# Kernel optimization log

Hardware: AMD Instinct MI355X
Metric: run time of the kernel (lower is better)

Reference implementation:

```python
import jax, jax.numpy as jnp
import numpy as np

B, T, C, H = 8, 2048, 1024, 1024
SCALE = 1.0 / np.sqrt(H).astype(np.float32)


def setup_inputs() -> dict:
    key = jax.random.key(0)
    kx, kq, kk, kv = jax.random.split(key, 4)
    x = jax.random.normal(kx, (B, T, C), dtype=jnp.float32)
    # Linear(C -> H, bias=False): store weights as [C, H] so y = x @ W
    Wq = jax.random.normal(kq, (C, H), dtype=jnp.float32) * (1.0 / np.sqrt(C))
    Wk = jax.random.normal(kk, (C, H), dtype=jnp.float32) * (1.0 / np.sqrt(C))
    Wv = jax.random.normal(kv, (C, H), dtype=jnp.float32) * (1.0 / np.sqrt(C))
    return {"x": x, "Wq": Wq, "Wk": Wk, "Wv": Wv}


def reference(x, Wq, Wk, Wv):
    # Projections
    Q = jnp.einsum('btc,ch->bth', x, Wq)
    K = jnp.einsum('btc,ch->bth', x, Wk)
    V = jnp.einsum('btc,ch->bth', x, Wv)
    t = x.shape[1]
    # Scaled dot-product scores with causal mask
    attn = jnp.einsum('bqh,bkh->bqk', Q, K) * SCALE  # [B,T,T]
    causal = jnp.tril(jnp.ones((t, t), dtype=bool))
    attn = jnp.where(causal, attn, -jnp.inf)
    scores = jax.nn.softmax(attn, axis=-1)
    # dropout p=0.0 (eval/deterministic) -> identity
    out = jnp.einsum('bqk,bkh->bqh', scores, V)
    return out
```

## Files before the change

kernel.cpp:

```cpp
#include <hip/hip_runtime.h>


#define BM 128
#define BN 128
#define BK 32

typedef __attribute__((ext_vector_type(8))) __bf16 bf16x8;
typedef __attribute__((ext_vector_type(4))) float floatx4;

__device__ __forceinline__ unsigned short f2bf(float f) {
  unsigned int u = __float_as_uint(f);
  u += 0x7fffu + ((u >> 16) & 1u);
  return (unsigned short)(u >> 16);
}
__device__ __forceinline__ float bf2f(unsigned short s) {
  return __uint_as_float(((unsigned int)s) << 16);
}

__device__ __forceinline__ void gload_lds16(const unsigned short* g, unsigned short* l) {
  __builtin_amdgcn_global_load_lds(
      (const __attribute__((address_space(1))) void*)g,
      (__attribute__((address_space(3))) void*)l,
      16, 0, 0);
}


__device__ __forceinline__ void gemm_mainloop(
    const unsigned short* __restrict__ A, int lda,
    const unsigned short* __restrict__ Bt, int ldb,
    int m0, int n0, int kTiles,
    unsigned short* As, unsigned short* Bs,
    floatx4 (&acc)[4][4])
{
  const int tid  = threadIdx.x;
  const int wave = tid >> 6;
  const int lane = tid & 63;
  const int wr = wave >> 1;
  const int wc = wave & 1;

  const int c0 = wave * 2;
  const int c1 = c0 + 1;
  const int r0 = c0 * 16 + (lane >> 2);
  const int r1 = c1 * 16 + (lane >> 2);
  const int ck = (lane & 3) * 8;

  const unsigned short* pA0 = A  + (size_t)(m0 + r0) * lda + ck;
  const unsigned short* pA1 = A  + (size_t)(m0 + r1) * lda + ck;
  const unsigned short* pB0 = Bt + (size_t)(n0 + r0) * ldb + ck;
  const unsigned short* pB1 = Bt + (size_t)(n0 + r1) * ldb + ck;

  unsigned short* lA0 = As + c0 * 512;
  unsigned short* lA1 = As + c1 * 512;
  unsigned short* lB0 = Bs + c0 * 512;
  unsigned short* lB1 = Bs + c1 * 512;

  const int fr = lane & 15;
  const int kq = (lane >> 4) * 8;

  for (int kt = 0; kt < kTiles; ++kt) {
    __syncthreads();
    gload_lds16(pA0, lA0);
    gload_lds16(pA1, lA1);
    gload_lds16(pB0, lB0);
    gload_lds16(pB1, lB1);
    pA0 += BK; pA1 += BK; pB0 += BK; pB1 += BK;
    __syncthreads();

    bf16x8 af[4], bg[4];
#pragma unroll
    for (int i = 0; i < 4; ++i)
      af[i] = *(const bf16x8*)(As + ((wr * 64 + i * 16 + fr) * BK + kq));
#pragma unroll
    for (int j = 0; j < 4; ++j)
      bg[j] = *(const bf16x8*)(Bs + ((wc * 64 + j * 16 + fr) * BK + kq));
#pragma unroll
    for (int i = 0; i < 4; ++i)
#pragma unroll
      for (int j = 0; j < 4; ++j)
        acc[i][j] = __builtin_amdgcn_mfma_f32_16x16x32_bf16(af[i], bg[j], acc[i][j], 0, 0, 0);
  }
}

#define ACC_INIT(acc)                         \
  do {                                        \
    floatx4 z_ = {0.f, 0.f, 0.f, 0.f};        \
    _Pragma("unroll")                         \
    for (int i_ = 0; i_ < 4; ++i_)            \
      _Pragma("unroll")                       \
      for (int j_ = 0; j_ < 4; ++j_)          \
        acc[i_][j_] = z_;                     \
  } while (0)


__global__ void cvt_x_kernel(const float* __restrict__ x, unsigned short* __restrict__ xb) {
  int idx = (blockIdx.x * 256 + threadIdx.x) * 4;
  float4 v = *(const float4*)(x + idx);
  ushort4 o;
  o.x = f2bf(v.x); o.y = f2bf(v.y); o.z = f2bf(v.z); o.w = f2bf(v.w);
  *(ushort4*)(xb + idx) = o;
}

__global__ void cvt_w_kernel(const float* __restrict__ W, unsigned short* __restrict__ Wt) {
  __shared__ unsigned short tile[64][65];
  const int k0 = blockIdx.x * 64, n0 = blockIdx.y * 64;
  const int tid = threadIdx.x, tx = tid & 63, ty = tid >> 6;
#pragma unroll
  for (int r = 0; r < 64; r += 4)
    tile[r + ty][tx] = f2bf(W[(size_t)(k0 + r + ty) * 1024 + (n0 + tx)]);
  __syncthreads();
#pragma unroll
  for (int r = 0; r < 64; r += 4)
    Wt[(size_t)(n0 + r + ty) * 1024 + (k0 + tx)] = tile[tx][r + ty];
}

__global__ void zero_l_kernel(float* __restrict__ l) {
  l[blockIdx.x * 256 + threadIdx.x] = 0.f;
}

__global__ __launch_bounds__(512, 2) void gemm_qkv_kernel(
    const unsigned short* __restrict__ xb,
    const unsigned short* __restrict__ Wt,
    unsigned short* __restrict__ Q,
    unsigned short* __restrict__ K,
    unsigned short* __restrict__ V)
{
  __shared__ __align__(16) unsigned short lds[49152];

  const int bid = blockIdx.x;
  const int lin = (bid & 7) * 96 + (bid >> 3);
  const int ni = lin >> 6;
  const int mi = lin & 63;
  const int m0 = mi * 256;
  const int n0 = ni * 256;

  const int tid = threadIdx.x;
  const int w = tid >> 6;
  const int l = tid & 63;
  const int wr = w >> 2;
  const int wc = w & 3;

  const int sr0 = w * 16 + (l >> 2);
  const int sr1 = 128 + sr0;
  const int sc  = l & 3;
  const int scs = ((sc ^ (sr0 & 3)) << 3);

  const unsigned short* pA0 = xb + (size_t)(m0 + sr0) * 1024 + scs;
  const unsigned short* pA1 = xb + (size_t)(m0 + sr1) * 1024 + scs;
  const unsigned short* pB0 = Wt + (size_t)(n0 + sr0) * 1024 + scs;
  const unsigned short* pB1 = Wt + (size_t)(n0 + sr1) * 1024 + scs;

  const int stgW = w * 512;

#define QKV_STAGE(slot)                                          \
  do {                                                           \
    unsigned short* _sA = &lds[(slot) * 8192 + stgW];            \
    unsigned short* _sB = &lds[24576 + (slot) * 8192 + stgW];    \
    gload_lds16(pA0, _sA);                                       \
    gload_lds16(pA1, _sA + 4096);                                \
    gload_lds16(pB0, _sB);                                       \
    gload_lds16(pB1, _sB + 4096);                                \
    pA0 += 32; pA1 += 32; pB0 += 32; pB1 += 32;                  \
  } while (0)

  const int fr = l & 15;
  const int q  = l >> 4;
  const int cks = (q ^ (fr & 3)) * 8;
  const int aOff = (wr * 128 + fr) * 32 + cks;
  const int bOff = (wc * 64 + fr) * 32 + cks;

  floatx4 acc[8][4];
  {
    floatx4 z = {0.f, 0.f, 0.f, 0.f};
#pragma unroll
    for (int i = 0; i < 8; ++i)
#pragma unroll
      for (int j = 0; j < 4; ++j)
        acc[i][j] = z;
  }

  QKV_STAGE(0);
  QKV_STAGE(1);
  asm volatile("s_waitcnt vmcnt(4)" ::: "memory");
  __builtin_amdgcn_s_barrier();

  int curSlot = 0, swSlot = 2;
  for (int kt = 0; kt < 32; ++kt) {
    const unsigned short* sA = &lds[curSlot * 8192];
    const unsigned short* sB = &lds[24576 + curSlot * 8192];

    bf16x8 a[8], b[4];
#pragma unroll
    for (int i = 0; i < 8; ++i)
      a[i] = *(const bf16x8*)(sA + aOff + i * 512);
#pragma unroll
    for (int j = 0; j < 4; ++j)
      b[j] = *(const bf16x8*)(sB + bOff + j * 512);

    if (kt < 30) QKV_STAGE(swSlot);

    __builtin_amdgcn_s_setprio(1);
#pragma unroll
    for (int i = 0; i < 8; ++i)
#pragma unroll
      for (int j = 0; j < 4; ++j)
        acc[i][j] = __builtin_amdgcn_mfma_f32_16x16x32_bf16(a[i], b[j], acc[i][j], 0, 0, 0);
    __builtin_amdgcn_s_setprio(0);

    if (kt < 31) {
      if (kt < 30) asm volatile("s_waitcnt vmcnt(4)" ::: "memory");
      else         asm volatile("s_waitcnt vmcnt(0)" ::: "memory");
      __builtin_amdgcn_s_barrier();
    }
    curSlot = (curSlot == 2) ? 0 : curSlot + 1;
    swSlot  = (swSlot  == 2) ? 0 : swSlot  + 1;
  }
#undef QKV_STAGE

  unsigned short* const dsts[3] = {Q, K, V};
  unsigned short* D = dsts[n0 >> 10];
  const int ncol0 = n0 & 1023;

  const int rb = m0 + wr * 128 + (q << 2);
  const int cb = ncol0 + wc * 64 + fr;
#pragma unroll
  for (int i = 0; i < 8; ++i)
#pragma unroll
    for (int j = 0; j < 4; ++j)
#pragma unroll
      for (int r = 0; r < 4; ++r)
        D[(size_t)(rb + i * 16 + r) * 1024 + (cb + j * 16)] = f2bf(acc[i][j][r]);
}

__global__ void transpose_v_kernel(const unsigned short* __restrict__ V,
                                   unsigned short* __restrict__ Vt) {
  __shared__ unsigned short tile[64][68];
  const int b = blockIdx.z;
  const int t0 = blockIdx.x * 64, h0 = blockIdx.y * 64;
  const int tid = threadIdx.x;
  const int cx = (tid & 15) * 4;
  const int ry = tid >> 4;
  const unsigned short* Vb = V + (size_t)b * 2048 * 1024;
#pragma unroll
  for (int r = 0; r < 64; r += 16) {
    ushort4 v = *(const ushort4*)(Vb + (size_t)(t0 + r + ry) * 1024 + (h0 + cx));
    *(ushort4*)&tile[r + ry][cx] = v;
  }
  __syncthreads();
  unsigned short* Vtb = Vt + (size_t)b * 1024 * 2048;
#pragma unroll
  for (int r = 0; r < 64; r += 16) {
    const int h = r + ry;
    ushort4 o;
    o.x = tile[cx][h]; o.y = tile[cx + 1][h]; o.z = tile[cx + 2][h]; o.w = tile[cx + 3][h];
    *(ushort4*)(Vtb + (size_t)(h0 + h) * 2048 + (t0 + cx)) = o;
  }
}

__global__ __launch_bounds__(256) void gemm_scores_kernel(
    const unsigned short* __restrict__ Q,
    const unsigned short* __restrict__ K,
    unsigned short* __restrict__ S,
    float* __restrict__ lsum)
{
  const int b = blockIdx.x & 7;
  const int t = blockIdx.x >> 3;
  int mi = (int)((sqrtf(8.f * (float)t + 1.f) - 1.f) * 0.5f);
  while ((mi + 1) * (mi + 2) / 2 <= t) ++mi;
  while (mi * (mi + 1) / 2 > t) --mi;
  const int ni = t - mi * (mi + 1) / 2;
  const int m0 = mi * BM;
  const int n0 = ni * BN;

  __shared__ __align__(16) unsigned short As[BM * BK];
  __shared__ __align__(16) unsigned short Bs[BN * BK];
  floatx4 acc[4][4];
  ACC_INIT(acc);
  const unsigned short* Qb = Q + (size_t)b * 2048 * 1024;
  const unsigned short* Kb = K + (size_t)b * 2048 * 1024;
  gemm_mainloop(Qb, 1024, Kb, 1024, m0, n0, 1024 / BK, As, Bs, acc);

  unsigned short* Sb = S + (size_t)b * 2048 * 2048;
  float* lb = lsum + b * 2048;
  const int tid = threadIdx.x, wave = tid >> 6, lane = tid & 63;
  const int wr = wave >> 1, wc = wave & 1;
  const int rb = m0 + wr * 64 + ((lane >> 4) << 2);
  const int cb = n0 + wc * 64 + (lane & 15);

  float rsum[4][4];
#pragma unroll
  for (int i = 0; i < 4; ++i)
#pragma unroll
    for (int r = 0; r < 4; ++r)
      rsum[i][r] = 0.f;

#pragma unroll
  for (int i = 0; i < 4; ++i)
#pragma unroll
    for (int j = 0; j < 4; ++j)
#pragma unroll
      for (int r = 0; r < 4; ++r) {
        const int tq = rb + i * 16 + r;
        const int tk = cb + j * 16;
        float e = 0.f;
        if (tk <= tq) e = __expf(acc[i][j][r] * 0.03125f);
        const unsigned short h = f2bf(e);
        Sb[(size_t)tq * 2048 + tk] = h;
        rsum[i][r] += bf2f(h);
      }

#pragma unroll
  for (int off = 1; off < 16; off <<= 1)
#pragma unroll
    for (int i = 0; i < 4; ++i)
#pragma unroll
      for (int r = 0; r < 4; ++r)
        rsum[i][r] += __shfl_xor(rsum[i][r], off, 64);

  if ((lane & 15) == 0) {
#pragma unroll
    for (int i = 0; i < 4; ++i)
#pragma unroll
      for (int r = 0; r < 4; ++r)
        atomicAdd(&lb[rb + i * 16 + r], rsum[i][r]);
  }
}

__global__ __launch_bounds__(256) void gemm_pv_kernel(
    const unsigned short* __restrict__ S,
    const unsigned short* __restrict__ Vt,
    const float* __restrict__ lsum,
    float* __restrict__ out)
{
  const int b = blockIdx.x & 7;
  const int r2 = blockIdx.x >> 3;
  const int mi = 15 - (r2 >> 3);
  const int ni = r2 & 7;
  const int m0 = mi * BM;
  const int n0 = ni * BN;

  __shared__ __align__(16) unsigned short As[BM * BK];
  __shared__ __align__(16) unsigned short Bs[BN * BK];
  floatx4 acc[4][4];
  ACC_INIT(acc);
  const unsigned short* Pb = S  + (size_t)b * 2048 * 2048;
  const unsigned short* Vb = Vt + (size_t)b * 1024 * 2048;
  const int kTiles = m0 / BK + BM / BK;
  gemm_mainloop(Pb, 2048, Vb, 2048, m0, n0, kTiles, As, Bs, acc);

  float* Ob = out + (size_t)b * 2048 * 1024;
  const float* lb = lsum + b * 2048;
  const int tid = threadIdx.x, wave = tid >> 6, lane = tid & 63;
  const int wr = wave >> 1, wc = wave & 1;
  const int rb = m0 + wr * 64 + ((lane >> 4) << 2);
  const int cb = n0 + wc * 64 + (lane & 15);

  float inv[4][4];
#pragma unroll
  for (int i = 0; i < 4; ++i)
#pragma unroll
    for (int r = 0; r < 4; ++r)
      inv[i][r] = 1.0f / lb[rb + i * 16 + r];

#pragma unroll
  for (int i = 0; i < 4; ++i)
#pragma unroll
    for (int j = 0; j < 4; ++j)
#pragma unroll
      for (int r = 0; r < 4; ++r)
        Ob[(size_t)(rb + i * 16 + r) * 1024 + (cb + j * 16)] = acc[i][j][r] * inv[i][r];
}


extern "C" void kernel_launch(void* const* d_in, const int* in_sizes, int n_in,
                              void* d_out, int out_size, void* d_ws, size_t ws_size,
                              hipStream_t stream) {
  const float* x  = (const float*)d_in[0];
  const float* Wq = (const float*)d_in[1];
  const float* Wk = (const float*)d_in[2];
  const float* Wv = (const float*)d_in[3];
  float* out = (float*)d_out;

  char* ws = (char*)d_ws;
  unsigned short* xb  = (unsigned short*)(ws);
  unsigned short* Wt  = (unsigned short*)(ws + 33554432ull);
  unsigned short* Q   = (unsigned short*)(ws + 39845888ull);
  unsigned short* K   = (unsigned short*)(ws + 73400320ull);
  unsigned short* V   = (unsigned short*)(ws + 106954752ull);
  unsigned short* Vt  = (unsigned short*)(ws + 140509184ull);
  unsigned short* S   = (unsigned short*)(ws + 174063616ull);
  float*          l   = (float*)ws;

  cvt_x_kernel<<<16384, 256, 0, stream>>>(x, xb);
  dim3 gw(16, 16);
  cvt_w_kernel<<<gw, 256, 0, stream>>>(Wq, Wt);
  cvt_w_kernel<<<gw, 256, 0, stream>>>(Wk, Wt + 1024 * 1024);
  cvt_w_kernel<<<gw, 256, 0, stream>>>(Wv, Wt + 2 * 1024 * 1024);

  gemm_qkv_kernel<<<768, 512, 0, stream>>>(xb, Wt, Q, K, V);

  transpose_v_kernel<<<dim3(32, 16, 8), 256, 0, stream>>>(V, Vt);
  zero_l_kernel<<<64, 256, 0, stream>>>(l);
  gemm_scores_kernel<<<8 * 136, 256, 0, stream>>>(Q, K, S, l);
  gemm_pv_kernel<<<1024, 256, 0, stream>>>(S, Vt, l, out);
}
```

Baseline: 379.2 us.

## Interleave LDS reads, global-to-LDS loads and MFMAs in QKV GEMM main loop

Restructures the QKV projection GEMM loop into four phases per K-tile, each issuing a pair of A-fragment LDS reads and one global_load_lds before a block of MFMAs. B fragments are double-buffered across iterations so the next tile's operands are prefetched ahead of the last MFMA group. It also changes the block-to-tile mapping so each XCD owns a contiguous band of M rows, and alters the LDS swizzle pattern. The many extra s_barriers add synchronisation cost, and the new swizzle must stay consistent between the writer and reader offsets.

```diff
diff --git a/kernel.cpp b/kernel.cpp
--- a/kernel.cpp
+++ b/kernel.cpp
@@ -127,9 +127,10 @@
   __shared__ __align__(16) unsigned short lds[49152];
 
   const int bid = blockIdx.x;
-  const int lin = (bid & 7) * 96 + (bid >> 3);
-  const int ni = lin >> 6;
-  const int mi = lin & 63;
+  const int xcd = bid & 7;
+  const int local = bid >> 3;
+  const int mi = xcd * 8 + (local & 7);
+  const int ni = local >> 3;
   const int m0 = mi * 256;
   const int n0 = ni * 256;
 
@@ -140,18 +141,16 @@
   const int wc = w & 3;
 
   const int sr0 = w * 16 + (l >> 2);
-  const int sr1 = 128 + sr0;
-  const int sc  = l & 3;
-  const int scs = ((sc ^ (sr0 & 3)) << 3);
+  const int scs = (((l & 3) ^ ((l >> 3) & 3)) << 3);
 
   const unsigned short* pA0 = xb + (size_t)(m0 + sr0) * 1024 + scs;
-  const unsigned short* pA1 = xb + (size_t)(m0 + sr1) * 1024 + scs;
+  const unsigned short* pA1 = xb + (size_t)(m0 + 128 + sr0) * 1024 + scs;
   const unsigned short* pB0 = Wt + (size_t)(n0 + sr0) * 1024 + scs;
-  const unsigned short* pB1 = Wt + (size_t)(n0 + sr1) * 1024 + scs;
+  const unsigned short* pB1 = Wt + (size_t)(n0 + 128 + sr0) * 1024 + scs;
 
   const int stgW = w * 512;
 
-#define QKV_STAGE(slot)                                          \
+#define STAGE4(slot)                                             \
   do {                                                           \
     unsigned short* _sA = &lds[(slot) * 8192 + stgW];            \
     unsigned short* _sB = &lds[24576 + (slot) * 8192 + stgW];    \
@@ -164,7 +163,7 @@
 
   const int fr = l & 15;
   const int q  = l >> 4;
-  const int cks = (q ^ (fr & 3)) * 8;
+  const int cks = ((q ^ ((fr >> 1) & 3)) << 3);
   const int aOff = (wr * 128 + fr) * 32 + cks;
   const int bOff = (wc * 64 + fr) * 32 + cks;
 
@@ -178,43 +177,96 @@
         acc[i][j] = z;
   }
 
-  QKV_STAGE(0);
-  QKV_STAGE(1);
+  STAGE4(0);
+  STAGE4(1);
   asm volatile("s_waitcnt vmcnt(4)" ::: "memory");
   __builtin_amdgcn_s_barrier();
 
-  int curSlot = 0, swSlot = 2;
-  for (int kt = 0; kt < 32; ++kt) {
-    const unsigned short* sA = &lds[curSlot * 8192];
-    const unsigned short* sB = &lds[24576 + curSlot * 8192];
-
-    bf16x8 a[8], b[4];
-#pragma unroll
-    for (int i = 0; i < 8; ++i)
-      a[i] = *(const bf16x8*)(sA + aOff + i * 512);
-#pragma unroll
-    for (int j = 0; j < 4; ++j)
-      b[j] = *(const bf16x8*)(sB + bOff + j * 512);
-
-    if (kt < 30) QKV_STAGE(swSlot);
-
-    __builtin_amdgcn_s_setprio(1);
-#pragma unroll
-    for (int i = 0; i < 8; ++i)
-#pragma unroll
-      for (int j = 0; j < 4; ++j)
-        acc[i][j] = __builtin_amdgcn_mfma_f32_16x16x32_bf16(a[i], b[j], acc[i][j], 0, 0, 0);
-    __builtin_amdgcn_s_setprio(0);
-
-    if (kt < 31) {
-      if (kt < 30) asm volatile("s_waitcnt vmcnt(4)" ::: "memory");
-      else         asm volatile("s_waitcnt vmcnt(0)" ::: "memory");
-      __builtin_amdgcn_s_barrier();
-    }
-    curSlot = (curSlot == 2) ? 0 : curSlot + 1;
-    swSlot  = (swSlot  == 2) ? 0 : swSlot  + 1;
-  }
-#undef QKV_STAGE
+  bf16x8 a[8], b0[4], b1[4];
+  {
+    const unsigned short* sA = &lds[0];
+    const unsigned short* sB = &lds[24576];
+#pragma unroll
+    for (int j = 0; j < 4; ++j) b0[j] = *(const bf16x8*)(sB + bOff + j * 512);
+    a[0] = *(const bf16x8*)(sA + aOff);
+    a[1] = *(const bf16x8*)(sA + aOff + 512);
+  }
+
+#define MFMA_PAIR(I0, BU)                                                           \
+  do {                                                                              \
+    __builtin_amdgcn_s_setprio(1);                                                  \
+    _Pragma("unroll")                                                               \
+    for (int j = 0; j < 4; ++j) {                                                   \
+      acc[(I0)][j] =                                                                \
+          __builtin_amdgcn_mfma_f32_16x16x32_bf16(a[(I0)], BU[j], acc[(I0)][j], 0, 0, 0); \
+      acc[(I0) + 1][j] =                                                            \
+          __builtin_amdgcn_mfma_f32_16x16x32_bf16(a[(I0) + 1], BU[j], acc[(I0) + 1][j], 0, 0, 0); \
+    }                                                                               \
+    __builtin_amdgcn_s_setprio(0);                                                  \
+  } while (0)
+
+#define ITER(KT, BU, BP)                                                  \
+  do {                                                                    \
+    const int nslot = (slot == 2) ? 0 : slot + 1;                         \
+    const int sslot = (nslot == 2) ? 0 : nslot + 1;                       \
+    const unsigned short* sA  = &lds[slot * 8192];                        \
+    const unsigned short* sAn = &lds[nslot * 8192];                       \
+    const unsigned short* sBn = &lds[24576 + nslot * 8192];               \
+    unsigned short* dA = &lds[sslot * 8192 + stgW];                       \
+    unsigned short* dB = &lds[24576 + sslot * 8192 + stgW];               \
+    const bool doStage = ((KT) < 30);                                     \
+    const bool doNext  = ((KT) < 31);                                     \
+     \
+    a[2] = *(const bf16x8*)(sA + aOff + 2 * 512);                         \
+    a[3] = *(const bf16x8*)(sA + aOff + 3 * 512);                         \
+    if (doStage) gload_lds16(pA0, dA);                                    \
+    __builtin_amdgcn_s_barrier();                                         \
+    MFMA_PAIR(0, BU);                                                     \
+    __builtin_amdgcn_s_barrier();                                         \
+                \
+    a[4] = *(const bf16x8*)(sA + aOff + 4 * 512);                         \
+    a[5] = *(const bf16x8*)(sA + aOff + 5 * 512);                         \
+    if (doStage) gload_lds16(pA1, dA + 4096);                             \
+    __builtin_amdgcn_s_barrier();                                         \
+    MFMA_PAIR(2, BU);                                                     \
+    __builtin_amdgcn_s_barrier();                                         \
+                \
+    a[6] = *(const bf16x8*)(sA + aOff + 6 * 512);                         \
+    a[7] = *(const bf16x8*)(sA + aOff + 7 * 512);                         \
+    if (doStage) gload_lds16(pB0, dB);                                    \
+    __builtin_amdgcn_s_barrier();                                         \
+    MFMA_PAIR(4, BU);                                                     \
+    __builtin_amdgcn_s_barrier();                                         \
+    \
+    if (doNext) {                                                         \
+      if (doStage) asm volatile("s_waitcnt vmcnt(3)" ::: "memory");       \
+      else         asm volatile("s_waitcnt vmcnt(0)" ::: "memory");       \
+      __builtin_amdgcn_s_barrier();                                       \
+      _Pragma("unroll")                                                   \
+      for (int j = 0; j < 4; ++j)                                         \
+        BP[j] = *(const bf16x8*)(sBn + bOff + j * 512);                   \
+      a[0] = *(const bf16x8*)(sAn + aOff);                                \
+      a[1] = *(const bf16x8*)(sAn + aOff + 512);                          \
+    }                                                                     \
+    if (doStage) {                                                        \
+      gload_lds16(pB1, dB + 4096);                                       \
+      pA0 += 32; pA1 += 32; pB0 += 32; pB1 += 32;                         \
+    }                                                                     \
+    MFMA_PAIR(6, BU);                                                     \
+    __builtin_amdgcn_s_barrier();                                         \
+    slot = nslot;                                                         \
+  } while (0)
+
+  int slot = 0;
+#pragma unroll 1
+  for (int kt2 = 0; kt2 < 16; ++kt2) {
+    const int kt = kt2 * 2;
+    ITER(kt, b0, b1);
+    ITER(kt + 1, b1, b0);
+  }
+#undef ITER
+#undef MFMA_PAIR
+#undef STAGE4
 
   unsigned short* const dsts[3] = {Q, K, V};
   unsigned short* D = dsts[n0 >> 10];
```

New measurement: 378.7 us. Within noise of the previous version (-0.1%).
